# Kernel optimization log

Hardware: AMD Instinct MI355X
Metric: run time of the kernel (lower is better)

The kernel has to match this reference:

```python
import jax, jax.numpy as jnp
import numpy as np

B, S, D = 4, 4096, 768  # batch, seq_len, n_units
NEG = -1000000000.0      # masked_fill value from the torch source


def setup_inputs() -> dict:
    key = jax.random.key(0)
    ks = jax.random.split(key, 12)
    scale = 1.0 / np.sqrt(D)
    inp = {
        "query": jax.random.normal(ks[0], (B, S, D), jnp.float32),
        "key_": jax.random.normal(ks[1], (B, S, D), jnp.float32),
        "value": jax.random.normal(ks[2], (B, S, D), jnp.float32),
        # nn.Linear weights are [out, in]; forward computes x @ W.T + b
        "Wq": jax.random.normal(ks[3], (D, D), jnp.float32) * scale,
        "bq": jnp.zeros((D,), jnp.float32),
        "Wk": jax.random.normal(ks[4], (D, D), jnp.float32) * scale,
        "bk": jnp.zeros((D,), jnp.float32),
        "Wv": jax.random.normal(ks[5], (D, D), jnp.float32) * scale,
        "bv": jnp.zeros((D,), jnp.float32),
        "Wo": jax.random.normal(ks[6], (D, D), jnp.float32) * scale,
        "bo": jnp.zeros((D,), jnp.float32),
        # broadcastable causal mask [1, S, S]; 0 -> masked
        "mask": jnp.tril(jnp.ones((S, S), jnp.int32))[None, :, :],
    }
    return inp


def reference(query, key_, value, Wq, bq, Wk, bk, Wv, bv, Wo, bo, mask):
    # QKV projections (torch Linear: x @ W.T + b)
    q = jnp.einsum("bsd,ed->bse", query, Wq) + bq
    k = jnp.einsum("bsd,ed->bse", key_, Wk) + bk
    v = jnp.einsum("bsd,ed->bse", value, Wv) + bv
    # scores: NOTE source scales by n_units**0.5 (full model dim, no head split)
    weights = jnp.einsum("bqd,bkd->bqk", q, k) / jnp.sqrt(jnp.float32(D))
    weights = jnp.where(mask == 0, jnp.float32(NEG), weights)
    weights = jax.nn.softmax(weights, axis=-1)
    # dropout is identity in eval/deterministic reference
    attended = jnp.einsum("bqk,bkd->bqd", weights, v)
    return jnp.einsum("bsd,ed->bse", attended, Wo) + bo
```

## Files before the change

kernel.cpp:

```cpp
#include <hip/hip_runtime.h>
#include <hip/hip_bf16.h>
#include <stdint.h>

#define DI __device__ __forceinline__

typedef __bf16 bf16x4 __attribute__((ext_vector_type(4)));
typedef __bf16 bf16x8 __attribute__((ext_vector_type(8)));
typedef float  f32x4  __attribute__((ext_vector_type(4)));

static constexpr int  BATCH = 4;
static constexpr int  SEQ   = 4096;
static constexpr int  DIM   = 768;
static constexpr long TOK   = (long)BATCH * SEQ;
static constexpr int  QT    = SEQ / 128;
static constexpr int  NTRI  = QT * (QT + 1) / 2;
static constexpr float SCALE = 0.0360843918243516150f;

__global__ void cvt4_kernel(const float* __restrict__ a, const float* __restrict__ b,
                            const float* __restrict__ c, const float* __restrict__ d,
                            __bf16* __restrict__ oa, __bf16* __restrict__ ob,
                            __bf16* __restrict__ oc, __bf16* __restrict__ od, long n4){
  const float* in  = blockIdx.y == 0 ? a : blockIdx.y == 1 ? b : blockIdx.y == 2 ? c : d;
  __bf16*      out = blockIdx.y == 0 ? oa : blockIdx.y == 1 ? ob : blockIdx.y == 2 ? oc : od;
  long i = (long)blockIdx.x * blockDim.x + threadIdx.x;
  const long stride = (long)gridDim.x * blockDim.x;
  for(; i < n4; i += stride){
    float4 v = ((const float4*)in)[i];
    bf16x4 o = { (__bf16)v.x, (__bf16)v.y, (__bf16)v.z, (__bf16)v.w };
    ((bf16x4*)out)[i] = o;
  }
}

DI int swz_off(int r, int c){ return (r << 7) + ((c ^ (r & 7)) << 4); }

template<int R>
DI void stage(const __bf16* __restrict__ src, long ld, char* lds, int tid){
  const int w = tid >> 6, l = tid & 63;
  const int rsub = l >> 3;
  const int kc   = (l & 7) ^ rsub;
  const __bf16* g = src + (long)(w * 8 + rsub) * ld + kc * 8;
  char* d = lds + (w << 10);
  #pragma unroll
  for(int i = 0; i < R / 64; ++i){
    __builtin_amdgcn_global_load_lds(
        (const __attribute__((address_space(1))) void*)(g + (long)(i * 64) * ld),
        (__attribute__((address_space(3))) void*)(d + i * 8192), 16, 0, 0);
  }
}

template<int R>
DI void stage_cvt(const float* __restrict__ src, long ld, char* lds, int tid){
  const int w = tid >> 6, l = tid & 63;
  const int rsub = l >> 3;
  const int kc   = (l & 7) ^ rsub;
  const float* g = src + (long)(w * 8 + rsub) * ld + kc * 8;
  char* d = lds + (w << 10) + ((l & 63) << 4);
  #pragma unroll
  for(int i = 0; i < R / 64; ++i){
    const float4* s = (const float4*)(g + (long)(i * 64) * ld);
    float4 v0 = s[0], v1 = s[1];
    bf16x8 o = { (__bf16)v0.x, (__bf16)v0.y, (__bf16)v0.z, (__bf16)v0.w,
                 (__bf16)v1.x, (__bf16)v1.y, (__bf16)v1.z, (__bf16)v1.w };
    *(bf16x8*)(d + i * 8192) = o;
  }
}

DI bf16x8 frag_ld(const char* lds, int row, int c){
  return *(const bf16x8*)(lds + swz_off(row, c));
}

DI void mma_tile(const char* As, const char* Bs, int lane, int wr, int wc, f32x4 acc[4][4]){
  #pragma unroll
  for(int kk = 0; kk < 2; ++kk){
    const int c = kk * 4 + (lane >> 4);
    bf16x8 a[4], b[4];
    #pragma unroll
    for(int i = 0; i < 4; ++i) a[i] = frag_ld(As, wr + i * 16 + (lane & 15), c);
    #pragma unroll
    for(int j = 0; j < 4; ++j) b[j] = frag_ld(Bs, wc + j * 16 + (lane & 15), c);
    #pragma unroll
    for(int i = 0; i < 4; ++i)
      #pragma unroll
      for(int j = 0; j < 4; ++j)
        acc[i][j] = __builtin_amdgcn_mfma_f32_16x16x32_bf16(a[i], b[j], acc[i][j], 0, 0, 0);
  }
}

template<class FA, class FB>
DI void kloop2(FA fa, long lda, FB fb, long ldb, int nt, int tid,
               char* As, char* Bs, f32x4 acc[4][4]){
  const int lane = tid & 63, w = tid >> 6;
  const int wr = (w >> 2) * 64, wc = (w & 3) * 64;
  for(int t = 0; t < nt; ++t){
    stage<128>(fa(t), lda, As, tid);
    stage<256>(fb(t), ldb, Bs, tid);
    __syncthreads();
    mma_tile(As, Bs, lane, wr, wc, acc);
    __syncthreads();
  }
}

__global__ __launch_bounds__(512)
void proj_qk(const float* __restrict__ query, const float* __restrict__ key_,
             const __bf16* __restrict__ Wqb, const __bf16* __restrict__ Wkb,
             const float* __restrict__ bq, const float* __restrict__ bk,
             __bf16* __restrict__ qb, __bf16* __restrict__ kb){
  __shared__ __attribute__((aligned(128))) char As[16384];
  __shared__ __attribute__((aligned(128))) char Bs[32768];
  const int z = blockIdx.y, bid = blockIdx.x, tid = threadIdx.x;
  const float*  X = z ? key_ : query;
  const __bf16* W = z ? Wkb : Wqb;
  const float*  bias = z ? bk : bq;
  __bf16*       C = z ? kb : qb;
  const long m0 = (long)(bid / 3) * 128, n0 = (bid % 3) * 256;
  const float*  Ar = X + m0 * DIM;
  const __bf16* Br = W + n0 * DIM;
  f32x4 acc[4][4] = {};
  const int lane = tid & 63, w = tid >> 6;
  const int wr = (w >> 2) * 64, wc = (w & 3) * 64;
  for(int t = 0; t < DIM / 64; ++t){
    stage_cvt<128>(Ar + t * 64, DIM, As, tid);
    stage<256>(Br + t * 64, DIM, Bs, tid);
    __syncthreads();
    mma_tile(As, Bs, lane, wr, wc, acc);
    __syncthreads();
  }
  const int cl = lane & 15, rq = (lane >> 4) * 4;
  #pragma unroll
  for(int i = 0; i < 4; ++i)
    #pragma unroll
    for(int j = 0; j < 4; ++j){
      const long gc = n0 + wc + j * 16 + cl;
      #pragma unroll
      for(int e = 0; e < 4; ++e){
        const long gr = m0 + wr + i * 16 + rq + e;
        C[gr * DIM + gc] = (__bf16)(acc[i][j][e] + bias[gc]);
      }
    }
}

__global__ __launch_bounds__(512)
void proj_vT(const __bf16* __restrict__ Wvb, const float* __restrict__ value,
             const float* __restrict__ bv, __bf16* __restrict__ vbT){
  __shared__ __attribute__((aligned(128))) char As[16384];
  __shared__ __attribute__((aligned(128))) char Bs[32768];
  const int bid = blockIdx.x, tid = threadIdx.x;
  const long m0 = (long)(bid / 64) * 128, n0 = (long)(bid % 64) * 256;
  const __bf16* Ar = Wvb + m0 * DIM;
  const float*  Br = value + n0 * DIM;
  f32x4 acc[4][4] = {};
  const int lane = tid & 63, w = tid >> 6;
  const int wr = (w >> 2) * 64, wc = (w & 3) * 64;
  for(int t = 0; t < DIM / 64; ++t){
    stage<128>(Ar + t * 64, DIM, As, tid);
    stage_cvt<256>(Br + t * 64, DIM, Bs, tid);
    __syncthreads();
    mma_tile(As, Bs, lane, wr, wc, acc);
    __syncthreads();
  }
  const int cl = lane & 15, rq = (lane >> 4) * 4;
  #pragma unroll
  for(int i = 0; i < 4; ++i)
    #pragma unroll
    for(int j = 0; j < 4; ++j){
      const long gc = n0 + wc + j * 16 + cl;
      #pragma unroll
      for(int e = 0; e < 4; ++e){
        const long gr = m0 + wr + i * 16 + rq + e;
        vbT[gr * TOK + gc] = (__bf16)(acc[i][j][e] + bv[gr]);
      }
    }
}

__global__ __launch_bounds__(512)
void qk_kernel(const __bf16* __restrict__ qb, const __bf16* __restrict__ kb,
               __bf16* __restrict__ Pc, float* __restrict__ rlsum){
  const int b = blockIdx.y, t2 = blockIdx.x, tid = threadIdx.x;
  int Qi = (int)((sqrtf(4.0f * t2 + 1.0f) - 1.0f) * 0.5f);
  while((Qi + 1) * (Qi + 2) <= t2) Qi++;
  while(Qi * (Qi + 1) > t2) Qi--;
  const int ki = t2 - Qi * (Qi + 1);
  const __bf16* Aq = qb + ((long)b * SEQ + Qi * 256) * DIM;
  const __bf16* Bk = kb + ((long)b * SEQ + ki * 128) * DIM;
  __shared__ __attribute__((aligned(128))) char As[32768];
  __shared__ __attribute__((aligned(128))) char Bs[16384];
  const int lane = tid & 63, w = tid >> 6;
  const int wr = (w >> 1) * 64, wc = (w & 1) * 64;
  f32x4 acc[4][4] = {};
  for(int t = 0; t < DIM / 64; ++t){
    stage<256>(Aq + t * 64, DIM, As, tid);
    stage<128>(Bk + t * 64, DIM, Bs, tid);
    __syncthreads();
    mma_tile(As, Bs, lane, wr, wc, acc);
    __syncthreads();
  }
  const int cl = lane & 15, rq = (lane >> 4) * 4;
  #pragma unroll
  for(int i = 0; i < 4; ++i){
    const int rbase = wr + i * 16;
    const int qi = 2 * Qi + (rbase >> 7);
    if(ki > qi) continue;
    const bool diag = (ki == qi);
    __bf16* tile = Pc + ((long)b * NTRI + (long)qi * (qi + 1) / 2 + ki) * 16384;
    float rsum[4] = {0.f, 0.f, 0.f, 0.f};
    #pragma unroll
    for(int j = 0; j < 4; ++j){
      const int c = wc + j * 16 + cl;
      #pragma unroll
      for(int e = 0; e < 4; ++e){
        const int rloc = (rbase + rq + e) & 127;
        float p = (diag && c > rloc) ? 0.0f
                  : __expf(fminf(acc[i][j][e] * SCALE, 30.0f));
        tile[rloc * 128 + c] = (__bf16)p;
        rsum[e] += p;
      }
    }
    #pragma unroll
    for(int e = 0; e < 4; ++e){
      float s = rsum[e];
      s += __shfl_xor(s, 1); s += __shfl_xor(s, 2);
      s += __shfl_xor(s, 4); s += __shfl_xor(s, 8);
      if(cl == 0){
        const long gr = (long)b * SEQ + Qi * 256 + rbase + rq + e;
        atomicAdd(&rlsum[gr], s);
      }
    }
  }
}

__global__ __launch_bounds__(512)
void pv_kernel(const __bf16* __restrict__ Pc, const float* __restrict__ rlsum,
               const __bf16* __restrict__ vbT, __bf16* __restrict__ att){
  __shared__ __attribute__((aligned(128))) char As[16384];
  __shared__ __attribute__((aligned(128))) char Bs[32768];
  __shared__ float sRl[128];
  const int b = blockIdx.z, qi = 31 - blockIdx.y, tid = threadIdx.x;
  const long n0 = (long)blockIdx.x * 256;
  if(tid < 128) sRl[tid] = 1.0f / rlsum[b * SEQ + qi * 128 + tid];
  const __bf16* Pq = Pc + ((long)b * NTRI + (long)qi * (qi + 1) / 2) * 16384;
  const __bf16* Bv = vbT + n0 * TOK + (long)b * SEQ;
  f32x4 acc[4][4] = {};
  auto fa = [&](int t){ return Pq + (long)(t >> 1) * 16384 + (t & 1) * 64; };
  auto fb = [&](int t){ return Bv + t * 64; };
  kloop2(fa, 128, fb, TOK, 2 * (qi + 1), tid, As, Bs, acc);

  const int lane = tid & 63, w = tid >> 6;
  const int wr = (w >> 2) * 64, wc = (w & 3) * 64;
  const int cl = lane & 15, rq = (lane >> 4) * 4;
  #pragma unroll
  for(int i = 0; i < 4; ++i)
    #pragma unroll
    for(int j = 0; j < 4; ++j){
      const long gc = n0 + wc + j * 16 + cl;
      #pragma unroll
      for(int e = 0; e < 4; ++e){
        const int rloc = wr + i * 16 + rq + e;
        float v = acc[i][j][e] * sRl[rloc];
        att[((long)b * SEQ + qi * 128 + rloc) * DIM + gc] = (__bf16)v;
      }
    }
}

__global__ __launch_bounds__(512)
void oproj(const __bf16* __restrict__ att, const __bf16* __restrict__ Wob,
           const float* __restrict__ bo, float* __restrict__ out){
  __shared__ __attribute__((aligned(128))) char As[16384];
  __shared__ __attribute__((aligned(128))) char Bs[32768];
  const int bid = blockIdx.x, tid = threadIdx.x;
  const long n0 = (bid % 3) * 256, m0 = (long)(bid / 3) * 128;
  const __bf16* Ar = att + m0 * DIM;
  const __bf16* Br = Wob + n0 * DIM;
  f32x4 acc[4][4] = {};
  auto fa = [&](int t){ return Ar + t * 64; };
  auto fb = [&](int t){ return Br + t * 64; };
  kloop2(fa, DIM, fb, DIM, DIM / 64, tid, As, Bs, acc);
  const int lane = tid & 63, w = tid >> 6;
  const int wr = (w >> 2) * 64, wc = (w & 3) * 64;
  const int cl = lane & 15, rq = (lane >> 4) * 4;
  #pragma unroll
  for(int i = 0; i < 4; ++i)
    #pragma unroll
    for(int j = 0; j < 4; ++j){
      const long gc = n0 + wc + j * 16 + cl;
      #pragma unroll
      for(int e = 0; e < 4; ++e){
        const long gr = m0 + wr + i * 16 + rq + e;
        out[gr * DIM + gc] = acc[i][j][e] + bo[gc];
      }
    }
}

extern "C" void kernel_launch(void* const* d_in, const int* in_sizes, int n_in,
                              void* d_out, int out_size, void* d_ws, size_t ws_size,
                              hipStream_t stream){
  const float* query = (const float*)d_in[0];
  const float* key_  = (const float*)d_in[1];
  const float* value = (const float*)d_in[2];
  const float* Wq = (const float*)d_in[3];
  const float* bq = (const float*)d_in[4];
  const float* Wk = (const float*)d_in[5];
  const float* bk = (const float*)d_in[6];
  const float* Wv = (const float*)d_in[7];
  const float* bv = (const float*)d_in[8];
  const float* Wo = (const float*)d_in[9];
  const float* bo = (const float*)d_in[10];

  char* p = (char*)d_ws;
  auto carve = [&](size_t bytes)->char*{
    char* r = p; p += (bytes + 255) & ~(size_t)255; return r;
  };
  const size_t tb = (size_t)TOK * DIM * 2;
  __bf16* qb  = (__bf16*)carve(tb);
  __bf16* kb  = (__bf16*)carve(tb);
  __bf16* vbT = (__bf16*)carve(tb);
  __bf16* att = (__bf16*)carve(tb);
  __bf16* Wqb = (__bf16*)carve((size_t)DIM * DIM * 2);
  __bf16* Wkb = (__bf16*)carve((size_t)DIM * DIM * 2);
  __bf16* Wvb = (__bf16*)carve((size_t)DIM * DIM * 2);
  __bf16* Wob = (__bf16*)carve((size_t)DIM * DIM * 2);
  __bf16* Pc  = (__bf16*)carve((size_t)BATCH * NTRI * 16384 * 2);
  float*  rlr = (float*)carve((size_t)TOK * 4);
  if((size_t)(p - (char*)d_ws) > ws_size) return;

  const long nW4 = (long)DIM * DIM / 4;
  dim3 g4((unsigned)((nW4 + 255) / 256), 4);
  hipMemsetAsync(rlr, 0, (size_t)TOK * 4, stream);
  cvt4_kernel<<<g4, 256, 0, stream>>>(Wq, Wk, Wv, Wo, Wqb, Wkb, Wvb, Wob, nW4);

  proj_qk<<<dim3(384, 2), 512, 0, stream>>>(query, key_, Wqb, Wkb, bq, bk, qb, kb);
  proj_vT<<<384, 512, 0, stream>>>(Wvb, value, bv, vbT);

  qk_kernel<<<dim3(272, BATCH), 512, 0, stream>>>(qb, kb, Pc, rlr);

  pv_kernel<<<dim3(3, QT, BATCH), 512, 0, stream>>>(Pc, rlr, vbT, att);

  oproj<<<384, 512, 0, stream>>>(att, Wob, bo, (float*)d_out);
}
```

Measured before the change: 321.1 us.

## Split PV kernel along key dimension into two halves and merge QKV projections

The PV kernel's work per query tile is split into two key-range halves written to separate attention buffers. This balances the triangular causal workload across more blocks (12x63 grid instead of 3x32x4). The output projection sums the two partial buffers while staging its A operand. Q/K and V projections are fused into one launch with a third grid slice. The cost is an extra full-size buffer, a memset of it, and extra reads in the output projection, plus bf16 rounding of each partial sum before they are added.

Measured after the change: 315.7 us. No clear change (-1.7%).

```diff
diff --git a/kernel.cpp b/kernel.cpp
--- a/kernel.cpp
+++ b/kernel.cpp
@@ -54,7 +54,7 @@
   const int rsub = l >> 3;
   const int kc   = (l & 7) ^ rsub;
   const float* g = src + (long)(w * 8 + rsub) * ld + kc * 8;
-  char* d = lds + (w << 10) + ((l & 63) << 4);
+  char* d = lds + (w << 10) + (l << 4);
   #pragma unroll
   for(int i = 0; i < R / 64; ++i){
     const float4* s = (const float4*)(g + (long)(i * 64) * ld);
@@ -65,6 +65,25 @@
   }
 }
 
+template<int R>
+DI void stage_add(const __bf16* __restrict__ a0, const __bf16* __restrict__ a1,
+                  long ld, char* lds, int tid){
+  const int w = tid >> 6, l = tid & 63;
+  const int rsub = l >> 3;
+  const int kc   = (l & 7) ^ rsub;
+  const long off = (long)(w * 8 + rsub) * ld + kc * 8;
+  char* d = lds + (w << 10) + (l << 4);
+  #pragma unroll
+  for(int i = 0; i < R / 64; ++i){
+    bf16x8 v0 = *(const bf16x8*)(a0 + off + (long)(i * 64) * ld);
+    bf16x8 v1 = *(const bf16x8*)(a1 + off + (long)(i * 64) * ld);
+    bf16x8 o;
+    #pragma unroll
+    for(int e = 0; e < 8; ++e) o[e] = (__bf16)((float)v0[e] + (float)v1[e]);
+    *(bf16x8*)(d + i * 8192) = o;
+  }
+}
+
 DI bf16x8 frag_ld(const char* lds, int row, int c){
   return *(const bf16x8*)(lds + swz_off(row, c));
 }
@@ -101,75 +120,69 @@
 }
 
 __global__ __launch_bounds__(512)
-void proj_qk(const float* __restrict__ query, const float* __restrict__ key_,
-             const __bf16* __restrict__ Wqb, const __bf16* __restrict__ Wkb,
-             const float* __restrict__ bq, const float* __restrict__ bk,
-             __bf16* __restrict__ qb, __bf16* __restrict__ kb){
+void proj_qkv(const float* __restrict__ query, const float* __restrict__ key_,
+              const float* __restrict__ value, const __bf16* __restrict__ Wqb,
+              const __bf16* __restrict__ Wkb, const __bf16* __restrict__ Wvb,
+              const float* __restrict__ bq, const float* __restrict__ bk,
+              const float* __restrict__ bv, __bf16* __restrict__ qb,
+              __bf16* __restrict__ kb, __bf16* __restrict__ vbT){
   __shared__ __attribute__((aligned(128))) char As[16384];
   __shared__ __attribute__((aligned(128))) char Bs[32768];
   const int z = blockIdx.y, bid = blockIdx.x, tid = threadIdx.x;
-  const float*  X = z ? key_ : query;
-  const __bf16* W = z ? Wkb : Wqb;
-  const float*  bias = z ? bk : bq;
-  __bf16*       C = z ? kb : qb;
-  const long m0 = (long)(bid / 3) * 128, n0 = (bid % 3) * 256;
-  const float*  Ar = X + m0 * DIM;
-  const __bf16* Br = W + n0 * DIM;
+  const int lane = tid & 63, w = tid >> 6;
+  const int wr = (w >> 2) * 64, wc = (w & 3) * 64;
   f32x4 acc[4][4] = {};
-  const int lane = tid & 63, w = tid >> 6;
-  const int wr = (w >> 2) * 64, wc = (w & 3) * 64;
-  for(int t = 0; t < DIM / 64; ++t){
-    stage_cvt<128>(Ar + t * 64, DIM, As, tid);
-    stage<256>(Br + t * 64, DIM, Bs, tid);
-    __syncthreads();
-    mma_tile(As, Bs, lane, wr, wc, acc);
-    __syncthreads();
-  }
   const int cl = lane & 15, rq = (lane >> 4) * 4;
-  #pragma unroll
-  for(int i = 0; i < 4; ++i)
-    #pragma unroll
-    for(int j = 0; j < 4; ++j){
-      const long gc = n0 + wc + j * 16 + cl;
-      #pragma unroll
-      for(int e = 0; e < 4; ++e){
-        const long gr = m0 + wr + i * 16 + rq + e;
-        C[gr * DIM + gc] = (__bf16)(acc[i][j][e] + bias[gc]);
-      }
-    }
-}
-
-__global__ __launch_bounds__(512)
-void proj_vT(const __bf16* __restrict__ Wvb, const float* __restrict__ value,
-             const float* __restrict__ bv, __bf16* __restrict__ vbT){
-  __shared__ __attribute__((aligned(128))) char As[16384];
-  __shared__ __attribute__((aligned(128))) char Bs[32768];
-  const int bid = blockIdx.x, tid = threadIdx.x;
-  const long m0 = (long)(bid / 64) * 128, n0 = (long)(bid % 64) * 256;
-  const __bf16* Ar = Wvb + m0 * DIM;
-  const float*  Br = value + n0 * DIM;
-  f32x4 acc[4][4] = {};
-  const int lane = tid & 63, w = tid >> 6;
-  const int wr = (w >> 2) * 64, wc = (w & 3) * 64;
-  for(int t = 0; t < DIM / 64; ++t){
-    stage<128>(Ar + t * 64, DIM, As, tid);
-    stage_cvt<256>(Br + t * 64, DIM, Bs, tid);
-    __syncthreads();
-    mma_tile(As, Bs, lane, wr, wc, acc);
-    __syncthreads();
-  }
-  const int cl = lane & 15, rq = (lane >> 4) * 4;
-  #pragma unroll
-  for(int i = 0; i < 4; ++i)
-    #pragma unroll
-    for(int j = 0; j < 4; ++j){
-      const long gc = n0 + wc + j * 16 + cl;
-      #pragma unroll
-      for(int e = 0; e < 4; ++e){
-        const long gr = m0 + wr + i * 16 + rq + e;
-        vbT[gr * TOK + gc] = (__bf16)(acc[i][j][e] + bv[gr]);
-      }
-    }
+
+  if(z < 2){
+    const float*  X = z ? key_ : query;
+    const __bf16* W = z ? Wkb : Wqb;
+    const float*  bias = z ? bk : bq;
+    __bf16*       C = z ? kb : qb;
+    const long m0 = (long)(bid / 3) * 128, n0 = (bid % 3) * 256;
+    const float*  Ar = X + m0 * DIM;
+    const __bf16* Br = W + n0 * DIM;
+    for(int t = 0; t < DIM / 64; ++t){
+      stage_cvt<128>(Ar + t * 64, DIM, As, tid);
+      stage<256>(Br + t * 64, DIM, Bs, tid);
+      __syncthreads();
+      mma_tile(As, Bs, lane, wr, wc, acc);
+      __syncthreads();
+    }
+    #pragma unroll
+    for(int i = 0; i < 4; ++i)
+      #pragma unroll
+      for(int j = 0; j < 4; ++j){
+        const long gc = n0 + wc + j * 16 + cl;
+        #pragma unroll
+        for(int e = 0; e < 4; ++e){
+          const long gr = m0 + wr + i * 16 + rq + e;
+          C[gr * DIM + gc] = (__bf16)(acc[i][j][e] + bias[gc]);
+        }
+      }
+  } else {
+    const long m0 = (long)(bid / 64) * 128, n0 = (long)(bid % 64) * 256;
+    const __bf16* Ar = Wvb + m0 * DIM;
+    const float*  Br = value + n0 * DIM;
+    for(int t = 0; t < DIM / 64; ++t){
+      stage<128>(Ar + t * 64, DIM, As, tid);
+      stage_cvt<256>(Br + t * 64, DIM, Bs, tid);
+      __syncthreads();
+      mma_tile(As, Bs, lane, wr, wc, acc);
+      __syncthreads();
+    }
+    #pragma unroll
+    for(int i = 0; i < 4; ++i)
+      #pragma unroll
+      for(int j = 0; j < 4; ++j){
+        const long gc = n0 + wc + j * 16 + cl;
+        #pragma unroll
+        for(int e = 0; e < 4; ++e){
+          const long gr = m0 + wr + i * 16 + rq + e;
+          vbT[gr * TOK + gc] = (__bf16)(acc[i][j][e] + bv[gr]);
+        }
+      }
+  }
 }
 
 __global__ __launch_bounds__(512)
@@ -230,20 +243,30 @@
 
 __global__ __launch_bounds__(512)
 void pv_kernel(const __bf16* __restrict__ Pc, const float* __restrict__ rlsum,
-               const __bf16* __restrict__ vbT, __bf16* __restrict__ att){
+               const __bf16* __restrict__ vbT, __bf16* __restrict__ att0,
+               __bf16* __restrict__ att1){
   __shared__ __attribute__((aligned(128))) char As[16384];
   __shared__ __attribute__((aligned(128))) char Bs[32768];
   __shared__ float sRl[128];
-  const int b = blockIdx.z, qi = 31 - blockIdx.y, tid = threadIdx.x;
-  const long n0 = (long)blockIdx.x * 256;
+  const int x = blockIdx.x, y = blockIdx.y, tid = threadIdx.x;
+  const long n0 = (long)(x >> 2) * 256;
+  const int b = x & 3;
+  int qi, k0, k1, half;
+  if(y == 62){ qi = 0; k0 = 0; k1 = 1; half = 0; }
+  else{
+    qi = 31 - (y >> 1); half = y & 1;
+    const int c0 = (qi + 2) >> 1;
+    if(half == 0){ k0 = 0; k1 = c0; } else { k0 = c0; k1 = qi + 1; }
+  }
   if(tid < 128) sRl[tid] = 1.0f / rlsum[b * SEQ + qi * 128 + tid];
   const __bf16* Pq = Pc + ((long)b * NTRI + (long)qi * (qi + 1) / 2) * 16384;
   const __bf16* Bv = vbT + n0 * TOK + (long)b * SEQ;
   f32x4 acc[4][4] = {};
-  auto fa = [&](int t){ return Pq + (long)(t >> 1) * 16384 + (t & 1) * 64; };
-  auto fb = [&](int t){ return Bv + t * 64; };
-  kloop2(fa, 128, fb, TOK, 2 * (qi + 1), tid, As, Bs, acc);
-
+  auto fa = [&](int t){ return Pq + (long)(k0 + (t >> 1)) * 16384 + (t & 1) * 64; };
+  auto fb = [&](int t){ return Bv + (long)k0 * 128 + t * 64; };
+  kloop2(fa, 128, fb, TOK, 2 * (k1 - k0), tid, As, Bs, acc);
+
+  __bf16* dst = half ? att1 : att0;
   const int lane = tid & 63, w = tid >> 6;
   const int wr = (w >> 2) * 64, wc = (w & 3) * 64;
   const int cl = lane & 15, rq = (lane >> 4) * 4;
@@ -256,26 +279,30 @@
       for(int e = 0; e < 4; ++e){
         const int rloc = wr + i * 16 + rq + e;
         float v = acc[i][j][e] * sRl[rloc];
-        att[((long)b * SEQ + qi * 128 + rloc) * DIM + gc] = (__bf16)v;
+        dst[((long)b * SEQ + qi * 128 + rloc) * DIM + gc] = (__bf16)v;
       }
     }
 }
 
 __global__ __launch_bounds__(512)
-void oproj(const __bf16* __restrict__ att, const __bf16* __restrict__ Wob,
-           const float* __restrict__ bo, float* __restrict__ out){
+void oproj(const __bf16* __restrict__ att0, const __bf16* __restrict__ att1,
+           const __bf16* __restrict__ Wob, const float* __restrict__ bo,
+           float* __restrict__ out){
   __shared__ __attribute__((aligned(128))) char As[16384];
   __shared__ __attribute__((aligned(128))) char Bs[32768];
   const int bid = blockIdx.x, tid = threadIdx.x;
   const long n0 = (bid % 3) * 256, m0 = (long)(bid / 3) * 128;
-  const __bf16* Ar = att + m0 * DIM;
   const __bf16* Br = Wob + n0 * DIM;
   f32x4 acc[4][4] = {};
-  auto fa = [&](int t){ return Ar + t * 64; };
-  auto fb = [&](int t){ return Br + t * 64; };
-  kloop2(fa, DIM, fb, DIM, DIM / 64, tid, As, Bs, acc);
   const int lane = tid & 63, w = tid >> 6;
   const int wr = (w >> 2) * 64, wc = (w & 3) * 64;
+  for(int t = 0; t < DIM / 64; ++t){
+    stage_add<128>(att0 + m0 * DIM + t * 64, att1 + m0 * DIM + t * 64, DIM, As, tid);
+    stage<256>(Br + t * 64, DIM, Bs, tid);
+    __syncthreads();
+    mma_tile(As, Bs, lane, wr, wc, acc);
+    __syncthreads();
+  }
   const int cl = lane & 15, rq = (lane >> 4) * 4;
   #pragma unroll
   for(int i = 0; i < 4; ++i)
@@ -310,10 +337,11 @@
     char* r = p; p += (bytes + 255) & ~(size_t)255; return r;
   };
   const size_t tb = (size_t)TOK * DIM * 2;
-  __bf16* qb  = (__bf16*)carve(tb);
-  __bf16* kb  = (__bf16*)carve(tb);
-  __bf16* vbT = (__bf16*)carve(tb);
-  __bf16* att = (__bf16*)carve(tb);
+  __bf16* qb   = (__bf16*)carve(tb);
+  __bf16* kb   = (__bf16*)carve(tb);
+  __bf16* vbT  = (__bf16*)carve(tb);
+  __bf16* att0 = (__bf16*)carve(tb);
+  __bf16* att1 = (__bf16*)carve(tb);
   __bf16* Wqb = (__bf16*)carve((size_t)DIM * DIM * 2);
   __bf16* Wkb = (__bf16*)carve((size_t)DIM * DIM * 2);
   __bf16* Wvb = (__bf16*)carve((size_t)DIM * DIM * 2);
@@ -325,14 +353,15 @@
   const long nW4 = (long)DIM * DIM / 4;
   dim3 g4((unsigned)((nW4 + 255) / 256), 4);
   hipMemsetAsync(rlr, 0, (size_t)TOK * 4, stream);
+  hipMemsetAsync(att1, 0, tb, stream);
   cvt4_kernel<<<g4, 256, 0, stream>>>(Wq, Wk, Wv, Wo, Wqb, Wkb, Wvb, Wob, nW4);
 
-  proj_qk<<<dim3(384, 2), 512, 0, stream>>>(query, key_, Wqb, Wkb, bq, bk, qb, kb);
-  proj_vT<<<384, 512, 0, stream>>>(Wvb, value, bv, vbT);
+  proj_qkv<<<dim3(384, 3), 512, 0, stream>>>(query, key_, value, Wqb, Wkb, Wvb,
+                                             bq, bk, bv, qb, kb, vbT);
 
   qk_kernel<<<dim3(272, BATCH), 512, 0, stream>>>(qb, kb, Pc, rlr);
 
-  pv_kernel<<<dim3(3, QT, BATCH), 512, 0, stream>>>(Pc, rlr, vbT, att);
-
-  oproj<<<384, 512, 0, stream>>>(att, Wob, bo, (float*)d_out);
-}
+  pv_kernel<<<dim3(12, 63), 512, 0, stream>>>(Pc, rlr, vbT, att0, att1);
+
+  oproj<<<384, 512, 0, stream>>>(att0, att1, Wob, bo, (float*)d_out);
+}
```
